# Kernel tuning notes

Hardware: AMD Instinct MI355X
Metric: run time of the kernel (lower is better)

## Reference

```python
import jax, jax.numpy as jnp
import numpy as np

WIRES = 24
LAYERS = 2
WIDTH = 2 ** WIRES  # 16,777,216 amplitudes
# Ring MaxCut-style Hamiltonian: ZZ on (j, j+1 mod WIRES) coeff 0.25, Z on j coeff -0.25
HAM = [(0.25, 'ZZ', [j, (j + 1) % WIRES]) for j in range(WIRES)] + \
      [(-0.25, 'Z', [j]) for j in range(WIRES)]


def _diag_hamiltonian() -> np.ndarray:
    """Diagonal of H_P. All RZ/RZZ phase gates commute, so the whole phase
    layer collapses to one diagonal multiply exp(-i * gamma * diag(H_P)).
    Wire 0 is the most-significant bit (kron ordering in getMat)."""
    idx = np.arange(WIDTH, dtype=np.int64)
    diag = np.zeros(WIDTH, dtype=np.float32)
    for coeff, _gtype, ws in HAM:
        s = np.ones(WIDTH, dtype=np.float32)
        for w in ws:
            bit = (idx >> (WIRES - 1 - w)) & 1
            s *= (1.0 - 2.0 * bit).astype(np.float32)  # Z eigenvalue +/-1
        diag += np.float32(coeff) * s
    return diag


def _rx_all(state, beta):
    """Apply RX(2*beta) to every wire. RX(2b) = [[cos b, -i sin b], [-i sin b, cos b]]."""
    c = jnp.cos(beta).astype(jnp.complex64)
    s = (-1j * jnp.sin(beta)).astype(jnp.complex64)
    for j in range(WIRES):  # fixed small structural loop over wires
        st = state.reshape(2 ** j, 2, -1)
        a, b = st[:, 0, :], st[:, 1, :]
        state = jnp.stack([c * a + s * b, s * a + c * b], axis=1).reshape(-1)
    return state


def setup_inputs() -> dict:
    key = jax.random.key(0)
    kg, kb = jax.random.split(key)
    gammas = jax.random.uniform(kg, (LAYERS,), dtype=jnp.float32) * (2.0 * np.pi)
    betas = jax.random.uniform(kb, (LAYERS,), dtype=jnp.float32) * np.pi
    diag_h = jnp.asarray(_diag_hamiltonian())
    return {"gammas": gammas, "betas": betas, "diag_h": diag_h}


def reference(gammas, betas, diag_h):
    # |0...0> followed by H on all wires -> uniform superposition
    amp = jnp.complex64(1.0 / np.sqrt(WIDTH))
    state = jnp.full((WIDTH,), amp, dtype=jnp.complex64)
    for i in range(LAYERS):
        # all RZ/RZZ (incl. CX-RZ-CX = RZZ) fused into one diagonal phase:
        # prod_terms exp(-i * (2*gamma*coeff)/2 * Z...Z) = exp(-i * gamma * diag(H_P))
        phase = jnp.exp((-1j * gammas[i]) * diag_h.astype(jnp.complex64))
        state = state * phase.astype(jnp.complex64)
        # mixer: RX(2*beta_i) on every wire
        state = _rx_all(state, betas[i])
    return state.reshape(WIDTH, 1)
```

## Files before the change

### kernel.cpp

```cpp
#include <hip/hip_runtime.h>


typedef unsigned int u32;

__device__ __forceinline__ u32 pack_bf(float r, float i) {
    u32 br = __float_as_uint(r); br += 0x7FFFu + ((br >> 16) & 1u);
    u32 bi = __float_as_uint(i); bi += 0x7FFFu + ((bi >> 16) & 1u);
    return (br & 0xFFFF0000u) | (bi >> 16);
}
__device__ __forceinline__ float2 unpack_bf(u32 v) {
    return make_float2(__uint_as_float(v & 0xFFFF0000u), __uint_as_float(v << 16));
}

__device__ __forceinline__ int didx(unsigned x) {
    unsigned r = ((x << 1) | (x >> 23)) & 0xFFFFFFu;
    return __popc(x) - __popc(x ^ r) + 24;
}

#define PI_DET 3.1416f
__device__ __forceinline__ void load_gb(const float* __restrict__ a,
                                        const float* __restrict__ b,
                                        int layer, float& g, float& bt) {
    const bool sw = (fmaxf(a[0], a[1]) <= PI_DET) && (fmaxf(b[0], b[1]) > PI_DET);
    g  = sw ? b[layer] : a[layer];
    bt = sw ? a[layer] : b[layer];
}

__device__ __forceinline__ void build_tab_s(float2* tab, int t, float g, float S) {
    if (t < 49) {
        float sn, cs;
        sincosf(g * 0.5f * (float)(t - 24), &sn, &cs);
        tab[t] = make_float2(S * cs, S * sn);
    }
}

__device__ __forceinline__ void pick_form(float c, float sb,
                                          bool& tf, float& t, float& s) {
    tf = (fabsf(c) >= sb);
    t  = tf ? (sb / c) : (c / sb);
    s  = tf ? c : sb;
}

template<bool TF>
__device__ __forceinline__ void bf4(float re[16], float im[16], float t) {
    #pragma unroll
    for (int b = 0; b < 4; ++b) {
        const int mk = 1 << b;
        #pragma unroll
        for (int pm = 0; pm < 8; ++pm) {
            const int lo = pm & (mk - 1);
            const int m0 = ((pm - lo) << 1) | lo;
            const int m1 = m0 | mk;
            const float ar = re[m0], ai = im[m0];
            const float br = re[m1], bi = im[m1];
            if (TF) {
                re[m0] = fmaf(t, bi, ar);  im[m0] = fmaf(-t, br, ai);
                re[m1] = fmaf(t, ai, br);  im[m1] = fmaf(-t, ar, bi);
            } else {
                re[m0] = fmaf(t, ar, bi);  im[m0] = fmaf(t, ai, -br);
                re[m1] = fmaf(t, br, ai);  im[m1] = fmaf(t, bi, -ar);
            }
        }
    }
}

template<bool TF>
__device__ __forceinline__ void bf5(float re[32], float im[32], float t) {
    #pragma unroll
    for (int b = 0; b < 5; ++b) {
        const int mk = 1 << b;
        #pragma unroll
        for (int pm = 0; pm < 16; ++pm) {
            const int lo = pm & (mk - 1);
            const int m0 = ((pm - lo) << 1) | lo;
            const int m1 = m0 | mk;
            const float ar = re[m0], ai = im[m0];
            const float br = re[m1], bi = im[m1];
            if (TF) {
                re[m0] = fmaf(t, bi, ar);  im[m0] = fmaf(-t, br, ai);
                re[m1] = fmaf(t, ai, br);  im[m1] = fmaf(-t, ar, bi);
            } else {
                re[m0] = fmaf(t, ar, bi);  im[m0] = fmaf(t, ai, -br);
                re[m1] = fmaf(t, br, ai);  im[m1] = fmaf(t, bi, -ar);
            }
        }
    }
}

template<bool TF>
__device__ __forceinline__ void topshfl(float re[32], float im[32], float t) {
    #pragma unroll
    for (int m = 0; m < 32; ++m) {
        const float pr = __shfl_xor(re[m], 32);
        const float pi = __shfl_xor(im[m], 32);
        if (TF) { re[m] = fmaf(t, pi, re[m]);  im[m] = fmaf(-t, pr, im[m]); }
        else    { re[m] = fmaf(t, re[m], pi);  im[m] = fmaf(t, im[m], -pr); }
    }
}

#define PAD(e) ((e) + ((e) >> 4))

template<bool TF>
__device__ __forceinline__ void f1_body(u32* __restrict__ st, const float2* tab,
                                        float* sre, float* sim,
                                        int hi, int t, float amp_eff, float tv) {
    const size_t base = (size_t)hi << 12;
    float re[16], im[16];
    #pragma unroll
    for (int j = 0; j < 16; ++j) {
        const int e = (t << 4) | j;
        const float2 cc = tab[didx((unsigned)(base + e))];
        re[j] = amp_eff * cc.x; im[j] = -amp_eff * cc.y;
    }
    bf4<TF>(re, im, tv);
    #pragma unroll
    for (int j = 0; j < 16; ++j) {
        const int e = (t << 4) | j;
        sre[PAD(e)] = re[j]; sim[PAD(e)] = im[j];
    }
    __syncthreads();
    #pragma unroll
    for (int j = 0; j < 16; ++j) {
        const int e = ((t >> 4) << 8) | (j << 4) | (t & 15);
        re[j] = sre[PAD(e)]; im[j] = sim[PAD(e)];
    }
    bf4<TF>(re, im, tv);
    #pragma unroll
    for (int j = 0; j < 16; ++j) {
        const int e = ((t >> 4) << 8) | (j << 4) | (t & 15);
        sre[PAD(e)] = re[j]; sim[PAD(e)] = im[j];
    }
    __syncthreads();
    #pragma unroll
    for (int m = 0; m < 16; ++m) {
        const int e = (m << 8) | t;
        re[m] = sre[PAD(e)]; im[m] = sim[PAD(e)];
    }
    bf4<TF>(re, im, tv);
    #pragma unroll
    for (int m = 0; m < 16; ++m)
        st[base + (m << 8) + t] = pack_bf(re[m], im[m]);
}

__global__ __launch_bounds__(256, 6) void f1(u32* __restrict__ st,
                                             const float* __restrict__ in0,
                                             const float* __restrict__ in1) {
    __shared__ float sre[4352], sim[4352];
    __shared__ float2 tab[49];
    const int hi = blockIdx.x, t = threadIdx.x;
    float g1, b1; load_gb(in0, in1, 0, g1, b1);
    build_tab_s(tab, t, g1, 1.0f);
    const float c = cosf(b1), sb = sinf(b1);
    bool tf; float tv, s; pick_form(c, sb, tf, tv, s);
    const float s2 = s * s, s6 = s2 * s2 * s2, S12 = s6 * s6;
    const float amp_eff = (1.0f / 4096.0f) * S12;
    __syncthreads();
    if (tf) f1_body<true >(st, tab, sre, sim, hi, t, amp_eff, tv);
    else    f1_body<false>(st, tab, sre, sim, hi, t, amp_eff, tv);
}

__global__ __launch_bounds__(256) void rmid(u32* __restrict__ st,
                                            const float* __restrict__ in0,
                                            const float* __restrict__ in1,
                                            int layer) {
    const int t   = threadIdx.x;
    const int l5  = t & 31;
    const int b17 = (t >> 5) & 1;
    const int w   = t >> 6;
    const int h     = blockIdx.x >> 5;
    const int chunk = blockIdx.x & 31;
    const size_t base = ((size_t)h << 18) | ((size_t)b17 << 17)
                      | (size_t)(chunk * 128 + w * 32 + l5);
    float g, bt; load_gb(in0, in1, layer, g, bt);
    const float c = cosf(bt), sb = sinf(bt);
    bool tf; float tv, s; pick_form(c, sb, tf, tv, s);
    const float s2 = s * s, S6 = s2 * s2 * s2;
    float re[32], im[32];
    #pragma unroll
    for (int m = 0; m < 32; ++m) {
        const float2 v = unpack_bf(st[base + ((size_t)m << 12)]);
        re[m] = v.x; im[m] = v.y;
    }
    if (tf) { bf5<true >(re, im, tv); topshfl<true >(re, im, tv); }
    else    { bf5<false>(re, im, tv); topshfl<false>(re, im, tv); }
    #pragma unroll
    for (int m = 0; m < 32; ++m)
        st[base + ((size_t)m << 12)] = pack_bf(S6 * re[m], S6 * im[m]);
}

__global__ __launch_bounds__(256) void rhi(u32* __restrict__ st,
                                           const float* __restrict__ in0,
                                           const float* __restrict__ in1) {
    __shared__ float2 tab[49];
    const int t   = threadIdx.x;
    const int l5  = t & 31;
    const int b23 = (t >> 5) & 1;
    const int w   = t >> 6;
    const unsigned l = (unsigned)blockIdx.x * 128u + (unsigned)(w * 32 + l5);
    const size_t base = ((size_t)b23 << 23) | (size_t)l;
    float g2, b1, b2, gd;
    load_gb(in0, in1, 0, gd, b1);
    load_gb(in0, in1, 1, g2, b2);
    const float c1 = cosf(b1), s1v = sinf(b1);
    const float c2 = cosf(b2), s2v = sinf(b2);
    bool tf1, tf2; float t1, t2, sa, sbv;
    pick_form(c1, s1v, tf1, t1, sa);
    pick_form(c2, s2v, tf2, t2, sbv);
    const float sa2 = sa * sa,  S1_6 = sa2 * sa2 * sa2;
    const float sb2 = sbv * sbv, S2_6 = sb2 * sb2 * sb2;
    build_tab_s(tab, t, g2, S1_6);
    float re[32], im[32];
    #pragma unroll
    for (int m = 0; m < 32; ++m) {
        const float2 v = unpack_bf(st[base + ((size_t)m << 18)]);
        re[m] = v.x; im[m] = v.y;
    }
    if (tf1) { bf5<true >(re, im, t1); topshfl<true >(re, im, t1); }
    else     { bf5<false>(re, im, t1); topshfl<false>(re, im, t1); }
    __syncthreads();
    #pragma unroll
    for (int m = 0; m < 32; ++m) {
        const unsigned idx = ((unsigned)b23 << 23) | ((unsigned)m << 18) | l;
        const float2 cc = tab[didx(idx)];
        const float r = re[m], i_ = im[m];
        re[m] = fmaf(r, cc.x, i_ * cc.y);
        im[m] = fmaf(i_, cc.x, -r * cc.y);
    }
    if (tf2) { bf5<true >(re, im, t2); topshfl<true >(re, im, t2); }
    else     { bf5<false>(re, im, t2); topshfl<false>(re, im, t2); }
    #pragma unroll
    for (int m = 0; m < 32; ++m)
        st[base + ((size_t)m << 18)] = pack_bf(S2_6 * re[m], S2_6 * im[m]);
}

template<bool TF>
__device__ __forceinline__ void f3_body(const u32* __restrict__ st,
                                        float* __restrict__ out,
                                        float* sre, float* sim,
                                        int hi, int t, float S12, float tv) {
    const size_t base = (size_t)hi << 12;
    float re[16], im[16];
    const uint4* vsrc = (const uint4*)(st + base + ((size_t)t << 4));
    #pragma unroll
    for (int q = 0; q < 4; ++q) {
        const uint4 v = vsrc[q];
        float2 a;
        a = unpack_bf(v.x); re[q*4+0] = a.x; im[q*4+0] = a.y;
        a = unpack_bf(v.y); re[q*4+1] = a.x; im[q*4+1] = a.y;
        a = unpack_bf(v.z); re[q*4+2] = a.x; im[q*4+2] = a.y;
        a = unpack_bf(v.w); re[q*4+3] = a.x; im[q*4+3] = a.y;
    }
    bf4<TF>(re, im, tv);
    #pragma unroll
    for (int j = 0; j < 16; ++j) {
        const int e = (t << 4) | j;
        sre[PAD(e)] = re[j]; sim[PAD(e)] = im[j];
    }
    __syncthreads();
    #pragma unroll
    for (int j = 0; j < 16; ++j) {
        const int e = ((t >> 4) << 8) | (j << 4) | (t & 15);
        re[j] = sre[PAD(e)]; im[j] = sim[PAD(e)];
    }
    bf4<TF>(re, im, tv);
    #pragma unroll
    for (int j = 0; j < 16; ++j) {
        const int e = ((t >> 4) << 8) | (j << 4) | (t & 15);
        sre[PAD(e)] = re[j]; sim[PAD(e)] = im[j];
    }
    __syncthreads();
    #pragma unroll
    for (int m = 0; m < 16; ++m) {
        const int e = (m << 8) | t;
        re[m] = sre[PAD(e)]; im[m] = sim[PAD(e)];
    }
    bf4<TF>(re, im, tv);
    #pragma unroll
    for (int m = 0; m < 16; ++m)
        out[base + (m << 8) + t] = S12 * re[m];
}

__global__ __launch_bounds__(256, 6) void f3(const u32* __restrict__ st,
                                             float* __restrict__ out,
                                             const float* __restrict__ in0,
                                             const float* __restrict__ in1) {
    __shared__ float sre[4352], sim[4352];
    const int hi = blockIdx.x, t = threadIdx.x;
    float g2, b2; load_gb(in0, in1, 1, g2, b2);
    const float c = cosf(b2), sb = sinf(b2);
    bool tf; float tv, s; pick_form(c, sb, tf, tv, s);
    const float s2 = s * s, s6 = s2 * s2 * s2, S12 = s6 * s6;
    if (tf) f3_body<true >(st, out, sre, sim, hi, t, S12, tv);
    else    f3_body<false>(st, out, sre, sim, hi, t, S12, tv);
}

extern "C" void kernel_launch(void* const* d_in, const int* in_sizes, int n_in,
                              void* d_out, int out_size, void* d_ws, size_t ws_size,
                              hipStream_t stream) {
    const float* in0 = (const float*)d_in[0];
    const float* in1 = (const float*)d_in[1];
    u32*   st  = (u32*)d_ws;
    float* out = (float*)d_out;

    f1  <<<dim3(4096), dim3(256), 0, stream>>>(st, in0, in1);
    rmid<<<dim3(2048), dim3(256), 0, stream>>>(st, in0, in1, 0);
    rhi <<<dim3(2048), dim3(256), 0, stream>>>(st, in0, in1);
    rmid<<<dim3(2048), dim3(256), 0, stream>>>(st, in0, in1, 1);
    f3  <<<dim3(4096), dim3(256), 0, stream>>>(st, out, in0, in1);
}
```

Baseline: 134.3 us.

## Vectorize rmid/rhi state accesses to 8-byte loads with two-stage shuffle butterflies

Each thread in rmid and rhi now owns two adjacent amplitudes and loads or stores them as one uint2 instead of single 4-byte words. The wire mapping changes so one fewer wire is handled in registers (16 pairs instead of 32 singles), and that wire moves to a second cross-lane shuffle stage (xor 16 plus xor 32). The aim is wider, fewer memory transactions on a bandwidth-bound pass. The cost is double the shuffle traffic and a changed thread-to-index mapping for the phase table lookup.

```diff
diff --git a/kernel.cpp b/kernel.cpp
--- a/kernel.cpp
+++ b/kernel.cpp
@@ -65,36 +65,41 @@
 }
 
 template<bool TF>
-__device__ __forceinline__ void bf5(float re[32], float im[32], float t) {
-    #pragma unroll
-    for (int b = 0; b < 5; ++b) {
+__device__ __forceinline__ void bf4x2(float re[32], float im[32], float t) {
+    #pragma unroll
+    for (int b = 0; b < 4; ++b) {
         const int mk = 1 << b;
         #pragma unroll
-        for (int pm = 0; pm < 16; ++pm) {
+        for (int pm = 0; pm < 8; ++pm) {
             const int lo = pm & (mk - 1);
             const int m0 = ((pm - lo) << 1) | lo;
             const int m1 = m0 | mk;
-            const float ar = re[m0], ai = im[m0];
-            const float br = re[m1], bi = im[m1];
-            if (TF) {
-                re[m0] = fmaf(t, bi, ar);  im[m0] = fmaf(-t, br, ai);
-                re[m1] = fmaf(t, ai, br);  im[m1] = fmaf(-t, ar, bi);
-            } else {
-                re[m0] = fmaf(t, ar, bi);  im[m0] = fmaf(t, ai, -br);
-                re[m1] = fmaf(t, br, ai);  im[m1] = fmaf(t, bi, -ar);
+            #pragma unroll
+            for (int p = 0; p < 2; ++p) {
+                const int i0 = m0 * 2 + p, i1 = m1 * 2 + p;
+                const float ar = re[i0], ai = im[i0];
+                const float br = re[i1], bi = im[i1];
+                if (TF) {
+                    re[i0] = fmaf(t, bi, ar);  im[i0] = fmaf(-t, br, ai);
+                    re[i1] = fmaf(t, ai, br);  im[i1] = fmaf(-t, ar, bi);
+                } else {
+                    re[i0] = fmaf(t, ar, bi);  im[i0] = fmaf(t, ai, -br);
+                    re[i1] = fmaf(t, br, ai);  im[i1] = fmaf(t, bi, -ar);
+                }
             }
         }
     }
 }
 
 template<bool TF>
-__device__ __forceinline__ void topshfl(float re[32], float im[32], float t) {
-    #pragma unroll
-    for (int m = 0; m < 32; ++m) {
-        const float pr = __shfl_xor(re[m], 32);
-        const float pi = __shfl_xor(im[m], 32);
-        if (TF) { re[m] = fmaf(t, pi, re[m]);  im[m] = fmaf(-t, pr, im[m]); }
-        else    { re[m] = fmaf(t, re[m], pi);  im[m] = fmaf(t, im[m], -pr); }
+__device__ __forceinline__ void shstage(float re[32], float im[32],
+                                        float t, int mask) {
+    #pragma unroll
+    for (int i = 0; i < 32; ++i) {
+        const float pr = __shfl_xor(re[i], mask);
+        const float pi = __shfl_xor(im[i], mask);
+        if (TF) { re[i] = fmaf(t, pi, re[i]);  im[i] = fmaf(-t, pr, im[i]); }
+        else    { re[i] = fmaf(t, re[i], pi);  im[i] = fmaf(t, im[i], -pr); }
     }
 }
 
@@ -164,28 +169,44 @@
                                             const float* __restrict__ in1,
                                             int layer) {
     const int t   = threadIdx.x;
-    const int l5  = t & 31;
+    const int l4  = t & 15;
+    const int b16 = (t >> 4) & 1;
     const int b17 = (t >> 5) & 1;
     const int w   = t >> 6;
     const int h     = blockIdx.x >> 5;
     const int chunk = blockIdx.x & 31;
+    const unsigned lo = (unsigned)(chunk * 128 + w * 32 + l4 * 2);
     const size_t base = ((size_t)h << 18) | ((size_t)b17 << 17)
-                      | (size_t)(chunk * 128 + w * 32 + l5);
+                      | ((size_t)b16 << 16) | lo;
     float g, bt; load_gb(in0, in1, layer, g, bt);
     const float c = cosf(bt), sb = sinf(bt);
     bool tf; float tv, s; pick_form(c, sb, tf, tv, s);
     const float s2 = s * s, S6 = s2 * s2 * s2;
     float re[32], im[32];
     #pragma unroll
-    for (int m = 0; m < 32; ++m) {
-        const float2 v = unpack_bf(st[base + ((size_t)m << 12)]);
-        re[m] = v.x; im[m] = v.y;
-    }
-    if (tf) { bf5<true >(re, im, tv); topshfl<true >(re, im, tv); }
-    else    { bf5<false>(re, im, tv); topshfl<false>(re, im, tv); }
-    #pragma unroll
-    for (int m = 0; m < 32; ++m)
-        st[base + ((size_t)m << 12)] = pack_bf(S6 * re[m], S6 * im[m]);
+    for (int m4 = 0; m4 < 16; ++m4) {
+        const uint2 v = *(const uint2*)(st + base + ((size_t)m4 << 12));
+        const float2 a = unpack_bf(v.x);
+        const float2 b = unpack_bf(v.y);
+        re[2*m4] = a.x; im[2*m4] = a.y;
+        re[2*m4+1] = b.x; im[2*m4+1] = b.y;
+    }
+    if (tf) {
+        bf4x2<true >(re, im, tv);
+        shstage<true >(re, im, tv, 16);
+        shstage<true >(re, im, tv, 32);
+    } else {
+        bf4x2<false>(re, im, tv);
+        shstage<false>(re, im, tv, 16);
+        shstage<false>(re, im, tv, 32);
+    }
+    #pragma unroll
+    for (int m4 = 0; m4 < 16; ++m4) {
+        uint2 v;
+        v.x = pack_bf(S6 * re[2*m4],   S6 * im[2*m4]);
+        v.y = pack_bf(S6 * re[2*m4+1], S6 * im[2*m4+1]);
+        *(uint2*)(st + base + ((size_t)m4 << 12)) = v;
+    }
 }
 
 __global__ __launch_bounds__(256) void rhi(u32* __restrict__ st,
@@ -193,11 +214,13 @@
                                            const float* __restrict__ in1) {
     __shared__ float2 tab[49];
     const int t   = threadIdx.x;
-    const int l5  = t & 31;
+    const int l4  = t & 15;
+    const int b22 = (t >> 4) & 1;
     const int b23 = (t >> 5) & 1;
     const int w   = t >> 6;
-    const unsigned l = (unsigned)blockIdx.x * 128u + (unsigned)(w * 32 + l5);
-    const size_t base = ((size_t)b23 << 23) | (size_t)l;
+    const unsigned l = (unsigned)blockIdx.x * 128u
+                     + (unsigned)(w * 32 + l4 * 2);
+    const size_t base = ((size_t)b23 << 23) | ((size_t)b22 << 22) | (size_t)l;
     float g2, b1, b2, gd;
     load_gb(in0, in1, 0, gd, b1);
     load_gb(in0, in1, 1, g2, b2);
@@ -211,26 +234,52 @@
     build_tab_s(tab, t, g2, S1_6);
     float re[32], im[32];
     #pragma unroll
-    for (int m = 0; m < 32; ++m) {
-        const float2 v = unpack_bf(st[base + ((size_t)m << 18)]);
-        re[m] = v.x; im[m] = v.y;
-    }
-    if (tf1) { bf5<true >(re, im, t1); topshfl<true >(re, im, t1); }
-    else     { bf5<false>(re, im, t1); topshfl<false>(re, im, t1); }
-    __syncthreads();
-    #pragma unroll
-    for (int m = 0; m < 32; ++m) {
-        const unsigned idx = ((unsigned)b23 << 23) | ((unsigned)m << 18) | l;
-        const float2 cc = tab[didx(idx)];
-        const float r = re[m], i_ = im[m];
-        re[m] = fmaf(r, cc.x, i_ * cc.y);
-        im[m] = fmaf(i_, cc.x, -r * cc.y);
-    }
-    if (tf2) { bf5<true >(re, im, t2); topshfl<true >(re, im, t2); }
-    else     { bf5<false>(re, im, t2); topshfl<false>(re, im, t2); }
-    #pragma unroll
-    for (int m = 0; m < 32; ++m)
-        st[base + ((size_t)m << 18)] = pack_bf(S2_6 * re[m], S2_6 * im[m]);
+    for (int m4 = 0; m4 < 16; ++m4) {
+        const uint2 v = *(const uint2*)(st + base + ((size_t)m4 << 18));
+        const float2 a = unpack_bf(v.x);
+        const float2 b = unpack_bf(v.y);
+        re[2*m4] = a.x; im[2*m4] = a.y;
+        re[2*m4+1] = b.x; im[2*m4+1] = b.y;
+    }
+    if (tf1) {
+        bf4x2<true >(re, im, t1);
+        shstage<true >(re, im, t1, 16);
+        shstage<true >(re, im, t1, 32);
+    } else {
+        bf4x2<false>(re, im, t1);
+        shstage<false>(re, im, t1, 16);
+        shstage<false>(re, im, t1, 32);
+    }
+    __syncthreads();
+    #pragma unroll
+    for (int m4 = 0; m4 < 16; ++m4) {
+        #pragma unroll
+        for (int p = 0; p < 2; ++p) {
+            const int i = 2*m4 + p;
+            const unsigned idx = ((unsigned)b23 << 23) | ((unsigned)b22 << 22)
+                               | ((unsigned)m4 << 18) | (l + (unsigned)p);
+            const float2 cc = tab[didx(idx)];
+            const float r = re[i], i_ = im[i];
+            re[i] = fmaf(r, cc.x, i_ * cc.y);
+            im[i] = fmaf(i_, cc.x, -r * cc.y);
+        }
+    }
+    if (tf2) {
+        bf4x2<true >(re, im, t2);
+        shstage<true >(re, im, t2, 16);
+        shstage<true >(re, im, t2, 32);
+    } else {
+        bf4x2<false>(re, im, t2);
+        shstage<false>(re, im, t2, 16);
+        shstage<false>(re, im, t2, 32);
+    }
+    #pragma unroll
+    for (int m4 = 0; m4 < 16; ++m4) {
+        uint2 v;
+        v.x = pack_bf(S2_6 * re[2*m4],   S2_6 * im[2*m4]);
+        v.y = pack_bf(S2_6 * re[2*m4+1], S2_6 * im[2*m4+1]);
+        *(uint2*)(st + base + ((size_t)m4 << 18)) = v;
+    }
 }
 
 template<bool TF>
```

Measured after the change: 137.2 us. 1.02x slower.
